# Optimization experiments

Measured on AMD Instinct MI355X. Metric: run time of the kernel, lower is better.

Reference implementation:

```python
import jax, jax.numpy as jnp
import numpy as np
from jax import lax

S, T = 128, 32768            # seq_len (tokens), token_size (samples per token)
K, STRIDE = 1024, 512        # kernel/fourier size, stride
HE, HD, C = 1024, 1024, 1024 # enc_hidden, dec_hidden, output classes
NW = (T - K) // STRIDE + 1   # 63 windows per token

_WIN_IDX = np.arange(NW)[:, None] * STRIDE + np.arange(K)  # (NW, K)

def strided_fourier(x):
    # x: (..., T) -> real part of FFT over each strided window: (..., NW, K)
    w = x[..., _WIN_IDX]
    return jnp.fft.fft(w, axis=-1).real.astype(x.dtype)

def _lstm_cell(h, c, gates, H):
    # torch gate order: i, f, g, o
    i = jax.nn.sigmoid(gates[..., 0:H])
    f = jax.nn.sigmoid(gates[..., H:2 * H])
    g = jnp.tanh(gates[..., 2 * H:3 * H])
    o = jax.nn.sigmoid(gates[..., 3 * H:4 * H])
    c = f * c + i * g
    h = o * jnp.tanh(c)
    return h, c


def setup_inputs() -> dict:
    key = jax.random.key(0)
    ks = jax.random.split(key, 13)
    def n(k, shape, s=0.02):
        return (jax.random.normal(k, shape, jnp.float32) * s)
    return {
        "x": jax.random.normal(ks[0], (S, T), jnp.float32),
        "Wih_e": n(ks[1], (4 * HE, K)), "Whh_e": n(ks[2], (4 * HE, HE)), "b_e": n(ks[3], (4 * HE,)),
        "Wm1": n(ks[4], (HE, HE)), "bm1": n(ks[5], (HE,)),
        "Wm2": n(ks[6], (HD, HE)), "bm2": n(ks[7], (HD,)),
        "Wih_d": n(ks[8], (4 * HD, K)), "Whh_d": n(ks[9], (4 * HD, HD)), "b_d": n(ks[10], (4 * HD,)),
        "Wo": n(ks[11], (C, HD)), "bo": n(ks[12], (C,)),
    }


def reference(x, Wih_e, Whh_e, b_e, Wm1, bm1, Wm2, bm2, Wih_d, Whh_d, b_d, Wo, bo):
    # --- strided FFT features (dropout=0 -> identity) ---
    fouriers = strided_fourier(x)  # (S, NW, K)

    # --- encoder LSTM: batch=S, time=NW ---
    def enc_step(carry, xt):  # xt: (S, K)
        h, c = carry
        gates = xt @ Wih_e.T + h @ Whh_e.T + b_e
        return _lstm_cell(h, c, gates, HE), None
    z = jnp.zeros((S, HE), x.dtype)
    (h_enc, _), _ = lax.scan(enc_step, (z, z), jnp.swapaxes(fouriers, 0, 1))

    # --- mid linear on final hidden: Linear->ReLU->Linear->Tanh ---
    h_mid = jnp.tanh(jax.nn.relu(h_enc @ Wm1.T + bm1) @ Wm2.T + bm2)  # (S, HD)
    h0 = h_mid[0]  # (HD,); torch code uses h for both h and c init

    # --- decoder: sequential over tokens, hidden carried across steps ---
    def outer(carry, fw):  # fw: (NW, K)
        def inner(hc, xt):  # xt: (K,)
            h, c = hc
            gates = xt @ Wih_d.T + h @ Whh_d.T + b_d
            return _lstm_cell(h, c, gates, HD), None
        (h, c), _ = lax.scan(inner, carry, fw)
        # dec_output[-1] == final hidden h
        out = jax.nn.log_softmax(h @ Wo.T + bo, axis=0)  # (C,)
        return (h, c), out

    _, outputs = lax.scan(outer, (h0, h0), fouriers)
    return outputs  # (S, C)
```

## Files before the change

kernel.cpp:

```cpp
#include <hip/hip_runtime.h>

typedef unsigned short u16;
typedef unsigned u32;
typedef unsigned long long u64;
typedef __bf16 bf16x8 __attribute__((ext_vector_type(8)));
typedef _Float16 half8 __attribute__((ext_vector_type(8)));
typedef _Float16 half2v __attribute__((ext_vector_type(2)));
typedef float f32x4 __attribute__((ext_vector_type(4)));
typedef unsigned uint4v __attribute__((ext_vector_type(4)));
typedef unsigned uint2v __attribute__((ext_vector_type(2)));

__device__ __forceinline__ u16 f2b(float f) {
  unsigned u = __builtin_bit_cast(unsigned, f);
  u = (u + 0x7FFFu + ((u >> 16) & 1u)) >> 16;
  return (u16)u;
}
__device__ __forceinline__ float b2f(u16 h) {
  return __builtin_bit_cast(float, ((unsigned)h) << 16);
}
__device__ __forceinline__ u16 f2h(float f) {
  _Float16 h = (_Float16)f;
  return __builtin_bit_cast(unsigned short, h);
}
__device__ __forceinline__ float sigmoidf_(float x) { return 1.0f / (1.0f + expf(-x)); }
__device__ __forceinline__ float fsig(float x) {
  x = fminf(fmaxf(x, -30.f), 30.f);
  return 1.0f / (1.0f + __expf(-x));
}
__device__ __forceinline__ float ftanh_(float x) {
  x = fminf(fmaxf(x, -15.f), 15.f);
  float e = __expf(2.0f * x);
  return (e - 1.0f) / (e + 1.0f);
}
__device__ __forceinline__ u64 aload(const u64* p) {
  return __hip_atomic_load(p, __ATOMIC_RELAXED, __HIP_MEMORY_SCOPE_AGENT);
}

__device__ __forceinline__ float fdot2_(u32 a, u32 b, float c) {
#if __has_builtin(__builtin_amdgcn_fdot2)
  return __builtin_amdgcn_fdot2(__builtin_bit_cast(half2v, a),
                                __builtin_bit_cast(half2v, b), c, false);
#else
  half2v x = __builtin_bit_cast(half2v, a), y = __builtin_bit_cast(half2v, b);
  return c + (float)x.x * (float)y.x + (float)x.y * (float)y.y;
#endif
}

__device__ __forceinline__ u64 l2_load1(const u64* p) {
  uint2v r;
  asm volatile("global_load_dwordx2 %0, %1, off sc0\n\ts_waitcnt vmcnt(0)"
               : "=&v"(r) : "v"(p) : "memory");
  return ((u64)r.y << 32) | (u64)r.x;
}
__device__ __forceinline__ void l2_store(u64* p, u64 v) {
  asm volatile("global_store_dwordx2 %0, %1, off" :: "v"(p), "v"(v) : "memory");
}

template <int EPI, bool OUTBF, bool ACC, bool SLAB = false>
__global__ __launch_bounds__(256) void gemm_bt(
    const u16* __restrict__ A, int lda,
    const u16* __restrict__ B, int ldb,
    void* __restrict__ Cout, int ldc,
    const float* __restrict__ bias,
    int M, int N, int K) {
  __shared__ __align__(16) u16 As[64 * 40];
  __shared__ __align__(16) u16 Bs[64 * 40];
  const int t = threadIdx.x;
  const int n0 = blockIdx.x * 64, m0 = blockIdx.y * 64;
  const int wave = t >> 6, lane = t & 63;
  const int wm = (wave >> 1) * 32, wn = (wave & 1) * 32;
  const int quad = lane >> 4, r16 = lane & 15;
  const int srow = t >> 2, scol = (t & 3) * 8;
  f32x4 acc[2][2] = {};
  const u16* ap = A + (size_t)(m0 + srow) * lda + scol;
  const u16* bp = B + (size_t)(n0 + srow) * ldb + scol;
  for (int k0 = 0; k0 < K; k0 += 32) {
    uint4 av = *(const uint4*)(ap + k0);
    uint4 bv = *(const uint4*)(bp + k0);
    __syncthreads();
    *(uint4*)&As[srow * 40 + scol] = av;
    *(uint4*)&Bs[srow * 40 + scol] = bv;
    __syncthreads();
    bf16x8 a0 = *(const bf16x8*)&As[(wm + r16) * 40 + quad * 8];
    bf16x8 a1 = *(const bf16x8*)&As[(wm + 16 + r16) * 40 + quad * 8];
    bf16x8 b0 = *(const bf16x8*)&Bs[(wn + r16) * 40 + quad * 8];
    bf16x8 b1 = *(const bf16x8*)&Bs[(wn + 16 + r16) * 40 + quad * 8];
    acc[0][0] = __builtin_amdgcn_mfma_f32_16x16x32_bf16(a0, b0, acc[0][0], 0, 0, 0);
    acc[0][1] = __builtin_amdgcn_mfma_f32_16x16x32_bf16(a0, b1, acc[0][1], 0, 0, 0);
    acc[1][0] = __builtin_amdgcn_mfma_f32_16x16x32_bf16(a1, b0, acc[1][0], 0, 0, 0);
    acc[1][1] = __builtin_amdgcn_mfma_f32_16x16x32_bf16(a1, b1, acc[1][1], 0, 0, 0);
  }
  for (int mi = 0; mi < 2; mi++)
    for (int ni = 0; ni < 2; ni++)
      for (int r = 0; r < 4; r++) {
        int gm = m0 + wm + mi * 16 + quad * 4 + r;
        int gn = n0 + wn + ni * 16 + r16;
        float v = acc[mi][ni][r];
        size_t idx;
        if (SLAB) {
          int q = gn >> 10, bb = (gn >> 5) & 31, jj = gn & 31;
          idx = ((size_t)bb * 8064 + gm) * 128 + q * 32 + jj;
        } else {
          idx = (size_t)gm * ldc + gn;
        }
        if (ACC) v += ((float*)Cout)[idx];
        if (bias) v += bias[gn];
        if (EPI == 1) v = fmaxf(v, 0.0f);
        if (EPI == 2) v = tanhf(v);
        if (OUTBF) ((u16*)Cout)[idx] = f2b(v);
        else ((float*)Cout)[idx] = v;
      }
}

__global__ __launch_bounds__(256) void k_cos(u16* __restrict__ Chi, u16* __restrict__ Clo) {
  int gid = blockIdx.x * 256 + threadIdx.x;
  int k = gid >> 10, n = gid & 1023;
  int m = (k * n) & 1023;
  float c = cospif((float)m * (1.0f / 512.0f));
  u16 hi = f2b(c);
  Chi[gid] = hi;
  Clo[gid] = f2b(c - b2f(hi));
}

__global__ __launch_bounds__(256) void k_win(const float* __restrict__ x,
                                             u16* __restrict__ Whi, u16* __restrict__ Wlo) {
  int gid = blockIdx.x * 256 + threadIdx.x;
  int e = gid * 4;
  int r = e >> 10, n = e & 1023;
  int wI = r >> 7, s = r & 127;
  const float* src = x + (size_t)s * 32768 + wI * 512 + n;
  float4 v = *(const float4*)src;
  float vv[4] = {v.x, v.y, v.z, v.w};
#pragma unroll
  for (int i = 0; i < 4; i++) {
    u16 hi = f2b(vv[i]);
    Whi[e + i] = hi;
    Wlo[e + i] = f2b(vv[i] - b2f(hi));
  }
}

__global__ __launch_bounds__(256) void k_f2bk(const float* __restrict__ src, u16* __restrict__ dst) {
  int gid = blockIdx.x * 256 + threadIdx.x;
  int i = gid * 4;
  float4 v = *(const float4*)(src + i);
  dst[i] = f2b(v.x); dst[i + 1] = f2b(v.y); dst[i + 2] = f2b(v.z); dst[i + 3] = f2b(v.w);
}

__global__ __launch_bounds__(256) void k_perm(const u16* __restrict__ F1, u16* __restrict__ F2) {
  int gid = blockIdx.x * 256 + threadIdx.x;
  int ro = gid >> 7, n8 = (gid & 127) * 8;
  int s = ro / 63, wI = ro % 63;
  *(uint4*)&F2[(size_t)ro * 1024 + n8] = *(const uint4*)&F1[(size_t)(wI * 128 + s) * 1024 + n8];
}

__global__ __launch_bounds__(256) void k_cell_enc(const float* __restrict__ g,
                                                  const u16* __restrict__ gihe, int t0,
                                                  float* __restrict__ c_e,
                                                  u16* __restrict__ At) {
  int gid = blockIdx.x * 256 + threadIdx.x;
  int s = gid >> 10, j = gid & 1023;
  const float* gr = g + (size_t)s * 4096;
  const u16* er = gihe + (size_t)(t0 * 128 + s) * 4096;
  float iv = sigmoidf_(gr[j] + b2f(er[j]));
  float fv = sigmoidf_(gr[j + 1024] + b2f(er[j + 1024]));
  float gv = tanhf(gr[j + 2048] + b2f(er[j + 2048]));
  float ov = sigmoidf_(gr[j + 3072] + b2f(er[j + 3072]));
  float c = fv * c_e[gid] + iv * gv;
  c_e[gid] = c;
  At[(size_t)s * 1024 + j] = f2b(ov * tanhf(c));
}

__global__ void k_initdec(const float* __restrict__ hmid, u64* __restrict__ hb,
                          int* __restrict__ ctrl, u64* __restrict__ probe,
                          u32* __restrict__ verdict) {
  int gid = blockIdx.x * blockDim.x + threadIdx.x;
  if (gid < 512) {
    u32 lo = (u32)f2h(hmid[2 * gid]) | ((u32)f2h(hmid[2 * gid + 1]) << 16);
    hb[gid] = (u64)lo;
  } else if (gid < 1024) {
    hb[gid] = 0xFFFFFFFF00000000ull;
  }
  if (gid < 9) ctrl[gid] = (gid == 8) ? -1 : 0;
  if (gid >= 16 && gid < 48) probe[gid - 16] = 0ull;
  if (gid >= 48 && gid < 80) verdict[gid - 48] = 0u;
}

__global__ __launch_bounds__(512, 2) void dec_persist(
    const float* __restrict__ Whh, const u16* __restrict__ GihS,
    const float* __restrict__ hmid,
    u64* __restrict__ hb, float* __restrict__ hfinal,
    int* __restrict__ ctrl, u64* __restrict__ probe, u32* __restrict__ verdict) {
  const int t = threadIdx.x;
  u32 xcd = __builtin_amdgcn_s_getreg(63508) & 7u;
  __shared__ int sslot;
  if (t == 0) {
    int tk = atomicAdd(&ctrl[xcd], 1);
    if (tk == 31) atomicCAS(&ctrl[8], -1, (int)xcd);
    int ch;
    do {
      ch = __hip_atomic_load(&ctrl[8], __ATOMIC_RELAXED, __HIP_MEMORY_SCOPE_AGENT);
    } while (ch < 0);
    sslot = (xcd == (u32)ch && tk < 32) ? tk : -1;
  }
  __syncthreads();
  const int b = sslot;
  if (b < 0) return;

  __shared__ int sok;
  if (t == 0) sok = 1;
  __syncthreads();
  for (int r = 0; r < 8; r++) {
    if (sok) {
      if (t == 0) l2_store(&probe[b], (u64)(0xC0DE0000u + (u32)r));
      if (t < 32) {
        const u64 want = (u64)(0xC0DE0000u + (u32)r);
        bool got = false;
        int lim = (r == 0) ? 30000 : 4000;
        for (int it = 0; it < lim; it++) {
          if (l2_load1(&probe[t]) >= want) { got = true; break; }
        }
        if (!got) sok = 0;
      }
    }
    __syncthreads();
  }
  if (t == 0)
    __hip_atomic_store(&verdict[b], sok ? 2u : 1u, __ATOMIC_RELAXED, __HIP_MEMORY_SCOPE_AGENT);
  __shared__ int modef;
  if (t == 0) modef = 2;
  __syncthreads();
  if (t < 32) {
    u32 v;
    do {
      v = __hip_atomic_load(&verdict[t], __ATOMIC_RELAXED, __HIP_MEMORY_SCOPE_AGENT);
    } while (v == 0);
    if (v != 2) atomicMin(&modef, 1);
  }
  __syncthreads();
  const bool fast = (modef == 2);

  const int w = t >> 6, lane = t & 63;
  const int quad = lane >> 4, r16 = lane & 15;
  const int hh = lane >> 5, jj = lane & 31;

  half8 afrag[2][4];
#pragma unroll
  for (int mt = 0; mt < 2; mt++) {
    int lr = mt * 16 + r16;
    const float* Wr = Whh + (size_t)(b * 32 + lr) * 1024 + 128 * w + quad * 8;
#pragma unroll
    for (int ks = 0; ks < 4; ks++) {
      half8 v;
#pragma unroll
      for (int j = 0; j < 8; j++) v[j] = (_Float16)Wr[ks * 32 + j];
      afrag[mt][ks] = v;
    }
  }
  u32 wv[3][32];
#pragma unroll
  for (int j = 0; j < 3; j++) {
    const float* Wr = Whh + (size_t)((j + 1) * 1024 + b * 32 + jj) * 1024 + 128 * w + 64 * hh;
#pragma unroll
    for (int i = 0; i < 16; i++) {
      float4 f = *(const float4*)(Wr + 4 * i);
      wv[j][2 * i]     = (u32)f2h(f.x) | ((u32)f2h(f.y) << 16);
      wv[j][2 * i + 1] = (u32)f2h(f.z) | ((u32)f2h(f.w) << 16);
    }
  }

  __shared__ __align__(16) u32 hsu[512];
  __shared__ __align__(16) float gpart[2][8][128];
  __shared__ __align__(16) u16 uslab[2][2048];

  {
    uint2v g0 = *(const uint2v*)(GihS + (size_t)b * 8064 * 128 + t * 4);
    *(uint2v*)&uslab[0][t * 4] = g0;
  }
  float cst = (t < 32) ? hmid[b * 32 + t] : 0.0f;

  int n = 0;
  for (int s = 0; s < 128; s++) {
    for (int wI = 0; wI < 63; wI++, n++) {
      const u32 tn = (u32)n;
      const u64* p = hb + (size_t)(n & 1) * 512 + t;
      u64 v;
      if (fast) {
        for (;;) {
          v = l2_load1(p);
          if ((u32)(v >> 32) == tn) break;
          __builtin_amdgcn_s_sleep(1);
        }
      } else {
        for (;;) {
          v = aload(p);
          if ((u32)(v >> 32) == tn) break;
        }
      }
      hsu[t] = (u32)v;

      const bool slabload = (n & 15) == 0;
      uint2v gsv;
      if (slabload) {
        int nn = (n + 16 <= 8048) ? n + 16 : 8048;
        gsv = *(const uint2v*)(GihS + ((size_t)b * 8064 + nn) * 128 + t * 4);
      }

      f32x4 acc0 = {0.f, 0.f, 0.f, 0.f}, acc1 = {0.f, 0.f, 0.f, 0.f};
      float accV[3] = {0.f, 0.f, 0.f};
#pragma unroll
      for (int g = 0; g < 4; g++) {
        half8 bfv = *(const half8*)&hsu[64 * w + 16 * g + 4 * quad];
        uint4v h0 = *(const uint4v*)&hsu[64 * w + 32 * hh + 8 * g];
        uint4v h1 = *(const uint4v*)&hsu[64 * w + 32 * hh + 8 * g + 4];
        acc0 = __builtin_amdgcn_mfma_f32_16x16x32_f16(afrag[0][g], bfv, acc0, 0, 0, 0);
        acc1 = __builtin_amdgcn_mfma_f32_16x16x32_f16(afrag[1][g], bfv, acc1, 0, 0, 0);
#pragma unroll
        for (int i2 = 0; i2 < 4; i2++)
#pragma unroll
          for (int j = 0; j < 3; j++)
            accV[j] = fdot2_(wv[j][8 * g + i2], h0[i2], accV[j]);
#pragma unroll
        for (int i2 = 0; i2 < 4; i2++)
#pragma unroll
          for (int j = 0; j < 3; j++)
            accV[j] = fdot2_(wv[j][8 * g + 4 + i2], h1[i2], accV[j]);
      }
      const int pb = n & 1;
      if (r16 == 0) {
        *(f32x4*)&gpart[pb][w][4 * quad] = acc0;
        *(f32x4*)&gpart[pb][w][16 + 4 * quad] = acc1;
      }
#pragma unroll
      for (int j = 0; j < 3; j++) {
        float sum = accV[j] + __shfl_xor(accV[j], 32);
        if (lane < 32) gpart[pb][w][32 + jj + 32 * j] = sum;
      }
      __syncthreads();
      if (slabload) *(uint2v*)&uslab[((n >> 4) + 1) & 1][t * 4] = gsv;
      if (w == 0) {
        const int sb = (n >> 4) & 1, so = (n & 15) * 128;
        const int rA = lane, rB = 64 + lane;
        float sA = 0.f, sB = 0.f;
#pragma unroll
        for (int ww = 0; ww < 8; ww++) {
          sA += gpart[pb][ww][rA];
          sB += gpart[pb][ww][rB];
        }
        sA += b2f(uslab[sb][so + rA]);
        sB += b2f(uslab[sb][so + rB]);
        float gA = fsig(sA);
        float gB = (lane < 32) ? ftanh_(sB) : fsig(sB);
        float fx = __shfl_xor(gA, 32);
        float ox = __shfl_xor(gB, 32);
        if (lane < 32) {
          cst = fx * cst + gA * gB;
          float h = ox * ftanh_(cst);
          u32 h16 = (u32)f2h(h);
          u32 oth = (u32)__shfl_down((int)h16, 1);
          if ((lane & 1) == 0) {
            u64 word = ((u64)(u32)(n + 1) << 32) | (h16 | (oth << 16));
            u64* dst = &hb[(size_t)((n + 1) & 1) * 512 + b * 16 + (lane >> 1)];
            if (fast) l2_store(dst, word);
            else __hip_atomic_store(dst, word, __ATOMIC_RELAXED, __HIP_MEMORY_SCOPE_AGENT);
          }
          if (wI == 62) hfinal[(size_t)s * 1024 + b * 32 + lane] = h;
        }
      }
    }
  }
}

__global__ __launch_bounds__(256) void k_lsm(const float* __restrict__ logits, float* __restrict__ out) {
  int s = blockIdx.x, t = threadIdx.x;
  const float* L = logits + (size_t)s * 1024;
  __shared__ float red[4], red2[4];
  float m = -1e30f;
  for (int i = t; i < 1024; i += 256) m = fmaxf(m, L[i]);
  for (int o = 1; o < 64; o <<= 1) m = fmaxf(m, __shfl_xor(m, o));
  if ((t & 63) == 0) red[t >> 6] = m;
  __syncthreads();
  m = fmaxf(fmaxf(red[0], red[1]), fmaxf(red[2], red[3]));
  float sum = 0.f;
  for (int i = t; i < 1024; i += 256) sum += expf(L[i] - m);
  for (int o = 1; o < 64; o <<= 1) sum += __shfl_xor(sum, o);
  if ((t & 63) == 0) red2[t >> 6] = sum;
  __syncthreads();
  sum = red2[0] + red2[1] + red2[2] + red2[3];
  float lse = m + logf(sum);
  for (int i = t; i < 1024; i += 256) out[(size_t)s * 1024 + i] = L[i] - lse;
}

extern "C" void kernel_launch(void* const* d_in, const int* in_sizes, int n_in,
                              void* d_out, int out_size, void* d_ws, size_t ws_size,
                              hipStream_t stream) {
  const float* x     = (const float*)d_in[0];
  const float* Wih_e = (const float*)d_in[1];
  const float* Whh_e = (const float*)d_in[2];
  const float* b_e   = (const float*)d_in[3];
  const float* Wm1   = (const float*)d_in[4];
  const float* bm1   = (const float*)d_in[5];
  const float* Wm2   = (const float*)d_in[6];
  const float* bm2   = (const float*)d_in[7];
  const float* Wih_d = (const float*)d_in[8];
  const float* Whh_d = (const float*)d_in[9];
  const float* b_d   = (const float*)d_in[10];
  const float* Wo    = (const float*)d_in[11];
  const float* bo    = (const float*)d_in[12];
  float* out = (float*)d_out;

  char* w = (char*)d_ws;
  size_t off = 0;
  auto alloc = [&](size_t bytes) { size_t r = off; off += (bytes + 255) & ~(size_t)255; return r; };
  u16* Chi = (u16*)(w + alloc((size_t)1024 * 1024 * 2));
  u16* Clo = (u16*)(w + alloc((size_t)1024 * 1024 * 2));
  u16* F1  = (u16*)(w + alloc((size_t)8064 * 1024 * 2));
  char* f2slot = w + alloc((size_t)8064 * 1024 * 2);
  u16* WinHi = (u16*)f2slot;
  u16* F2    = (u16*)f2slot;
  u16* WinLo = (u16*)(w + alloc((size_t)8064 * 1024 * 2));
  char* gislot = w + alloc((size_t)8064 * 4096 * 2);
  float* Fgem = (float*)gislot;
  u16* GihS   = (u16*)gislot;
  u16* Gihe = (u16*)(w + alloc((size_t)8064 * 4096 * 2));
  u16* Wihd  = (u16*)(w + alloc((size_t)4096 * 1024 * 2));
  u16* Wihe  = (u16*)(w + alloc((size_t)4096 * 1024 * 2));
  u16* Whhe  = (u16*)(w + alloc((size_t)4096 * 1024 * 2));
  u16* Wm1b = (u16*)(w + alloc((size_t)1024 * 1024 * 2));
  u16* Wm2b = (u16*)(w + alloc((size_t)1024 * 1024 * 2));
  u16* Wob  = (u16*)(w + alloc((size_t)1024 * 1024 * 2));
  u16* At   = (u16*)(w + alloc((size_t)128 * 1024 * 2));
  float* Ge = (float*)(w + alloc((size_t)128 * 4096 * 4));
  float* Ce = (float*)(w + alloc((size_t)128 * 1024 * 4));
  u16* Mid1 = (u16*)(w + alloc((size_t)128 * 1024 * 2));
  float* Hmid = (float*)(w + alloc((size_t)128 * 1024 * 4));
  u64* Hb = (u64*)(w + alloc((size_t)1024 * 8));
  int* Ctrl = (int*)(w + alloc(256));
  u64* Probe = (u64*)(w + alloc(256));
  u32* Verdict = (u32*)(w + alloc(256));
  float* Hfin = (float*)(w + alloc((size_t)128 * 1024 * 4));
  u16* Hfinb  = (u16*)(w + alloc((size_t)128 * 1024 * 2));
  float* Logit = (float*)(w + alloc((size_t)128 * 1024 * 4));
  (void)ws_size; (void)in_sizes; (void)n_in; (void)out_size;

  hipMemsetAsync(At, 0, (size_t)128 * 1024 * 2, stream);
  hipMemsetAsync(Ce, 0, (size_t)128 * 1024 * 4, stream);

  k_cos<<<4096, 256, 0, stream>>>(Chi, Clo);
  k_win<<<8064, 256, 0, stream>>>(x, WinHi, WinLo);
  gemm_bt<0, false, false><<<dim3(16, 126), 256, 0, stream>>>(WinHi, 1024, Chi, 1024, Fgem, 1024, nullptr, 8064, 1024, 1024);
  gemm_bt<0, false, true><<<dim3(16, 126), 256, 0, stream>>>(WinHi, 1024, Clo, 1024, Fgem, 1024, nullptr, 8064, 1024, 1024);
  gemm_bt<0, false, true><<<dim3(16, 126), 256, 0, stream>>>(WinLo, 1024, Chi, 1024, Fgem, 1024, nullptr, 8064, 1024, 1024);
  k_f2bk<<<8064, 256, 0, stream>>>(Fgem, F1);
  k_perm<<<4032, 256, 0, stream>>>(F1, F2);

  k_f2bk<<<4096, 256, 0, stream>>>(Wih_d, Wihd);
  k_f2bk<<<4096, 256, 0, stream>>>(Wih_e, Wihe);
  k_f2bk<<<4096, 256, 0, stream>>>(Whh_e, Whhe);
  k_f2bk<<<1024, 256, 0, stream>>>(Wm1, Wm1b);
  k_f2bk<<<1024, 256, 0, stream>>>(Wm2, Wm2b);
  k_f2bk<<<1024, 256, 0, stream>>>(Wo, Wob);

  gemm_bt<0, true, false, true><<<dim3(64, 126), 256, 0, stream>>>(F2, 1024, Wihd, 1024, GihS, 128, b_d, 8064, 4096, 1024);
  gemm_bt<0, true, false><<<dim3(64, 126), 256, 0, stream>>>(F1, 1024, Wihe, 1024, Gihe, 4096, b_e, 8064, 4096, 1024);

  for (int t = 0; t < 63; t++) {
    gemm_bt<0, false, false><<<dim3(64, 2), 256, 0, stream>>>(At, 1024, Whhe, 1024, Ge, 4096, nullptr, 128, 4096, 1024);
    k_cell_enc<<<512, 256, 0, stream>>>(Ge, Gihe, t, Ce, At);
  }

  gemm_bt<1, true, false><<<dim3(16, 2), 256, 0, stream>>>(At, 1024, Wm1b, 1024, Mid1, 1024, bm1, 128, 1024, 1024);
  gemm_bt<2, false, false><<<dim3(16, 2), 256, 0, stream>>>(Mid1, 1024, Wm2b, 1024, Hmid, 1024, bm2, 128, 1024, 1024);

  k_initdec<<<4, 256, 0, stream>>>(Hmid, Hb, Ctrl, Probe, Verdict);
  dec_persist<<<256, 512, 0, stream>>>(Whh_d, GihS, Hmid, Hb, Hfin, Ctrl, Probe, Verdict);

  k_f2bk<<<128, 256, 0, stream>>>(Hfin, Hfinb);
  gemm_bt<0, false, false><<<dim3(16, 2), 256, 0, stream>>>(Hfinb, 1024, Wob, 1024, Logit, 1024, bo, 128, 1024, 1024);
  k_lsm<<<128, 256, 0, stream>>>(Logit, out);
}
```

Baseline: 15.49 ms.

## Make each decoder wave independent with per-wave dot-products and no block barrier

Reworks the persistent decoder step so each wave owns 4 hidden units (all 16 gate rows) and computes them with fdot2 over the full 1024-length h vector loaded directly from global memory. Partial sums are reduced with a butterfly shuffle tree instead of LDS plus __syncthreads, which removes the per-step block barrier and the single-wave gate epilogue. Each lane now polls 64 bytes of the h buffer per step with wide sc0 loads. A large dummy LDS allocation is added that appears intended to limit occupancy. The change drops MFMA use and increases per-lane register weights and polling traffic.

```diff
diff --git a/kernel.cpp b/kernel.cpp
--- a/kernel.cpp
+++ b/kernel.cpp
@@ -191,6 +191,7 @@
     u64* __restrict__ hb, float* __restrict__ hfinal,
     int* __restrict__ ctrl, u64* __restrict__ probe, u32* __restrict__ verdict) {
   const int t = threadIdx.x;
+  __shared__ u32 lds_pad[19456];
   u32 xcd = __builtin_amdgcn_s_getreg(63508) & 7u;
   __shared__ int sslot;
   if (t == 0) {
@@ -204,6 +205,8 @@
   }
   __syncthreads();
   const int b = sslot;
+  if (__hip_atomic_load(&ctrl[8], __ATOMIC_RELAXED, __HIP_MEMORY_SCOPE_AGENT) == -2)
+    lds_pad[t] = (u32)t;
   if (b < 0) return;
 
   __shared__ int sok;
@@ -240,131 +243,135 @@
   const bool fast = (modef == 2);
 
   const int w = t >> 6, lane = t & 63;
-  const int quad = lane >> 4, r16 = lane & 15;
-  const int hh = lane >> 5, jj = lane & 31;
-
-  half8 afrag[2][4];
-#pragma unroll
-  for (int mt = 0; mt < 2; mt++) {
-    int lr = mt * 16 + r16;
-    const float* Wr = Whh + (size_t)(b * 32 + lr) * 1024 + 128 * w + quad * 8;
-#pragma unroll
-    for (int ks = 0; ks < 4; ks++) {
-      half8 v;
-#pragma unroll
-      for (int j = 0; j < 8; j++) v[j] = (_Float16)Wr[ks * 32 + j];
-      afrag[mt][ks] = v;
+
+  u32 wt[16][8];
+#pragma unroll
+  for (int r = 0; r < 16; r++) {
+    const float* Wr = Whh + (size_t)((r >> 2) * 1024 + b * 32 + w * 4 + (r & 3)) * 1024 + 16 * lane;
+#pragma unroll
+    for (int i = 0; i < 4; i++) {
+      float4 f = *(const float4*)(Wr + 4 * i);
+      wt[r][2 * i]     = (u32)f2h(f.x) | ((u32)f2h(f.y) << 16);
+      wt[r][2 * i + 1] = (u32)f2h(f.z) | ((u32)f2h(f.w) << 16);
     }
   }
-  u32 wv[3][32];
-#pragma unroll
-  for (int j = 0; j < 3; j++) {
-    const float* Wr = Whh + (size_t)((j + 1) * 1024 + b * 32 + jj) * 1024 + 128 * w + 64 * hh;
-#pragma unroll
-    for (int i = 0; i < 16; i++) {
-      float4 f = *(const float4*)(Wr + 4 * i);
-      wv[j][2 * i]     = (u32)f2h(f.x) | ((u32)f2h(f.y) << 16);
-      wv[j][2 * i + 1] = (u32)f2h(f.z) | ((u32)f2h(f.w) << 16);
-    }
-  }
-
-  __shared__ __align__(16) u32 hsu[512];
-  __shared__ __align__(16) float gpart[2][8][128];
-  __shared__ __align__(16) u16 uslab[2][2048];
-
+
+  __shared__ __align__(8) u16 uslabW[8][2][256];
   {
-    uint2v g0 = *(const uint2v*)(GihS + (size_t)b * 8064 * 128 + t * 4);
-    *(uint2v*)&uslab[0][t * 4] = g0;
-  }
-  float cst = (t < 32) ? hmid[b * 32 + t] : 0.0f;
+    int st = lane >> 2, g = lane & 3;
+    *(u64*)&uslabW[w][0][st * 16 + g * 4] =
+        *(const u64*)(GihS + ((size_t)b * 8064 + st) * 128 + g * 32 + w * 4);
+  }
+  float cst = (lane < 4) ? hmid[b * 32 + w * 4 + lane] : 0.0f;
 
   int n = 0;
   for (int s = 0; s < 128; s++) {
     for (int wI = 0; wI < 63; wI++, n++) {
       const u32 tn = (u32)n;
-      const u64* p = hb + (size_t)(n & 1) * 512 + t;
-      u64 v;
+      const u64* base = hb + (size_t)(n & 1) * 512 + 8 * lane;
+      u32 hreg[8];
       if (fast) {
         for (;;) {
-          v = l2_load1(p);
-          if ((u32)(v >> 32) == tn) break;
+          uint4v r0, r1, r2, r3;
+          asm volatile(
+              "global_load_dwordx4 %0, %4, off sc0\n\t"
+              "global_load_dwordx4 %1, %4, off offset:16 sc0\n\t"
+              "global_load_dwordx4 %2, %4, off offset:32 sc0\n\t"
+              "global_load_dwordx4 %3, %4, off offset:48 sc0\n\t"
+              "s_waitcnt vmcnt(0)"
+              : "=&v"(r0), "=&v"(r1), "=&v"(r2), "=&v"(r3)
+              : "v"(base) : "memory");
+          bool ok = (r0.y == tn) & (r0.w == tn) & (r1.y == tn) & (r1.w == tn) &
+                    (r2.y == tn) & (r2.w == tn) & (r3.y == tn) & (r3.w == tn);
+          if (ok) {
+            hreg[0] = r0.x; hreg[1] = r0.z; hreg[2] = r1.x; hreg[3] = r1.z;
+            hreg[4] = r2.x; hreg[5] = r2.z; hreg[6] = r3.x; hreg[7] = r3.z;
+            break;
+          }
           __builtin_amdgcn_s_sleep(1);
         }
       } else {
-        for (;;) {
-          v = aload(p);
-          if ((u32)(v >> 32) == tn) break;
-        }
-      }
-      hsu[t] = (u32)v;
+#pragma unroll
+        for (int i = 0; i < 8; i++) {
+          u64 v;
+          for (;;) {
+            v = aload(base + i);
+            if ((u32)(v >> 32) == tn) break;
+          }
+          hreg[i] = (u32)v;
+        }
+      }
 
       const bool slabload = (n & 15) == 0;
-      uint2v gsv;
+      u64 gsv;
       if (slabload) {
         int nn = (n + 16 <= 8048) ? n + 16 : 8048;
-        gsv = *(const uint2v*)(GihS + ((size_t)b * 8064 + nn) * 128 + t * 4);
-      }
-
-      f32x4 acc0 = {0.f, 0.f, 0.f, 0.f}, acc1 = {0.f, 0.f, 0.f, 0.f};
-      float accV[3] = {0.f, 0.f, 0.f};
-#pragma unroll
-      for (int g = 0; g < 4; g++) {
-        half8 bfv = *(const half8*)&hsu[64 * w + 16 * g + 4 * quad];
-        uint4v h0 = *(const uint4v*)&hsu[64 * w + 32 * hh + 8 * g];
-        uint4v h1 = *(const uint4v*)&hsu[64 * w + 32 * hh + 8 * g + 4];
-        acc0 = __builtin_amdgcn_mfma_f32_16x16x32_f16(afrag[0][g], bfv, acc0, 0, 0, 0);
-        acc1 = __builtin_amdgcn_mfma_f32_16x16x32_f16(afrag[1][g], bfv, acc1, 0, 0, 0);
-#pragma unroll
-        for (int i2 = 0; i2 < 4; i2++)
-#pragma unroll
-          for (int j = 0; j < 3; j++)
-            accV[j] = fdot2_(wv[j][8 * g + i2], h0[i2], accV[j]);
-#pragma unroll
-        for (int i2 = 0; i2 < 4; i2++)
-#pragma unroll
-          for (int j = 0; j < 3; j++)
-            accV[j] = fdot2_(wv[j][8 * g + 4 + i2], h1[i2], accV[j]);
-      }
-      const int pb = n & 1;
-      if (r16 == 0) {
-        *(f32x4*)&gpart[pb][w][4 * quad] = acc0;
-        *(f32x4*)&gpart[pb][w][16 + 4 * quad] = acc1;
-      }
-#pragma unroll
-      for (int j = 0; j < 3; j++) {
-        float sum = accV[j] + __shfl_xor(accV[j], 32);
-        if (lane < 32) gpart[pb][w][32 + jj + 32 * j] = sum;
-      }
-      __syncthreads();
-      if (slabload) *(uint2v*)&uslab[((n >> 4) + 1) & 1][t * 4] = gsv;
-      if (w == 0) {
-        const int sb = (n >> 4) & 1, so = (n & 15) * 128;
-        const int rA = lane, rB = 64 + lane;
-        float sA = 0.f, sB = 0.f;
-#pragma unroll
-        for (int ww = 0; ww < 8; ww++) {
-          sA += gpart[pb][ww][rA];
-          sB += gpart[pb][ww][rB];
-        }
-        sA += b2f(uslab[sb][so + rA]);
-        sB += b2f(uslab[sb][so + rB]);
-        float gA = fsig(sA);
-        float gB = (lane < 32) ? ftanh_(sB) : fsig(sB);
-        float fx = __shfl_xor(gA, 32);
-        float ox = __shfl_xor(gB, 32);
-        if (lane < 32) {
-          cst = fx * cst + gA * gB;
-          float h = ox * ftanh_(cst);
-          u32 h16 = (u32)f2h(h);
-          u32 oth = (u32)__shfl_down((int)h16, 1);
-          if ((lane & 1) == 0) {
-            u64 word = ((u64)(u32)(n + 1) << 32) | (h16 | (oth << 16));
-            u64* dst = &hb[(size_t)((n + 1) & 1) * 512 + b * 16 + (lane >> 1)];
-            if (fast) l2_store(dst, word);
-            else __hip_atomic_store(dst, word, __ATOMIC_RELAXED, __HIP_MEMORY_SCOPE_AGENT);
-          }
-          if (wI == 62) hfinal[(size_t)s * 1024 + b * 32 + lane] = h;
-        }
+        gsv = *(const u64*)(GihS + ((size_t)b * 8064 + nn + (lane >> 2)) * 128 +
+                            (lane & 3) * 32 + w * 4);
+      }
+
+      float v[16];
+#pragma unroll
+      for (int r = 0; r < 16; r++) {
+        float a0 = 0.f, a1 = 0.f;
+#pragma unroll
+        for (int i = 0; i < 4; i++) {
+          a0 = fdot2_(wt[r][2 * i], hreg[2 * i], a0);
+          a1 = fdot2_(wt[r][2 * i + 1], hreg[2 * i + 1], a1);
+        }
+        v[r] = a0 + a1;
+      }
+      if (slabload)
+        *(u64*)&uslabW[w][((n >> 4) + 1) & 1][(lane >> 2) * 16 + (lane & 3) * 4] = gsv;
+
+      {
+        const bool s1 = (lane & 1), s2 = (lane & 2), s4 = (lane & 4), s8 = (lane & 8);
+#pragma unroll
+        for (int i = 0; i < 8; i++) {
+          float keep = s1 ? v[2 * i + 1] : v[2 * i];
+          float send = s1 ? v[2 * i] : v[2 * i + 1];
+          v[i] = keep + __shfl_xor(send, 1);
+        }
+#pragma unroll
+        for (int i = 0; i < 4; i++) {
+          float keep = s2 ? v[2 * i + 1] : v[2 * i];
+          float send = s2 ? v[2 * i] : v[2 * i + 1];
+          v[i] = keep + __shfl_xor(send, 2);
+        }
+#pragma unroll
+        for (int i = 0; i < 2; i++) {
+          float keep = s4 ? v[2 * i + 1] : v[2 * i];
+          float send = s4 ? v[2 * i] : v[2 * i + 1];
+          v[i] = keep + __shfl_xor(send, 4);
+        }
+        {
+          float keep = s8 ? v[1] : v[0];
+          float send = s8 ? v[0] : v[1];
+          v[0] = keep + __shfl_xor(send, 8);
+        }
+        v[0] += __shfl_xor(v[0], 16);
+        v[0] += __shfl_xor(v[0], 32);
+      }
+
+      const int sb = (n >> 4) & 1;
+      const int r = lane & 15, g = r >> 2;
+      float sv = v[0] + b2f(uslabW[w][sb][(n & 15) * 16 + r]);
+      float act = (g == 2) ? ftanh_(sv) : fsig(sv);
+      float fv = __shfl(act, (lane & 3) + 4);
+      float gv = __shfl(act, (lane & 3) + 8);
+      float ov = __shfl(act, (lane & 3) + 12);
+      if (lane < 4) {
+        cst = fv * cst + act * gv;
+        float h = ov * ftanh_(cst);
+        u32 h16 = (u32)f2h(h);
+        u32 oth = (u32)__shfl_down((int)h16, 1);
+        if ((lane & 1) == 0) {
+          u64 word = ((u64)(u32)(n + 1) << 32) | (h16 | (oth << 16));
+          u64* dst = &hb[(size_t)((n + 1) & 1) * 512 + b * 16 + w * 2 + (lane >> 1)];
+          if (fast) l2_store(dst, word);
+          else __hip_atomic_store(dst, word, __ATOMIC_RELAXED, __HIP_MEMORY_SCOPE_AGENT);
+        }
+        if (wI == 62) hfinal[(size_t)s * 1024 + b * 32 + w * 4 + lane] = h;
       }
     }
   }
```

Result: slower. 61.32 ms (+295.9%).
